# Kernel tuning notes

Measured on AMD Instinct MI355X. Metric: run time of the kernel, lower is better.

Reference implementation:

```python
import jax, jax.numpy as jnp
import numpy as np

B, S, L = 64, 512, 768


def setup_inputs() -> dict:
    key = jax.random.key(0)
    k1, k2 = jax.random.split(key)
    x = jax.random.normal(k1, (B, S, L), dtype=jnp.float32)
    # matches torch uniform_(-0.1, 0.1) init for the probe matrix b
    b = jax.random.uniform(k2, (L, L), minval=-0.1, maxval=0.1, dtype=jnp.float32)
    return {"x": x, "b": b}


def reference(x, b):
    # Original: z[b,i,j,h] = x_i - x_j; h = einsum('gh,bijh', b, z); dist = sum_g h^2
    # Identity: ||b @ (x_i - x_j)||^2 = ||p_i||^2 + ||p_j||^2 - 2 p_i . p_j,  p = x @ b^T
    p = jnp.einsum('gh,bsh->bsg', b, x)          # [B, S, L] projected points
    sq = jnp.sum(p * p, axis=-1)                 # [B, S]  squared norms
    gram = jnp.einsum('bsg,btg->bst', p, p)      # [B, S, S] inner products
    return sq[:, :, None] + sq[:, None, :] - 2.0 * gram  # [B, S, S]
```

## Files before the change

### kernel.cpp

```cpp
#include <hip/hip_runtime.h>
#include <hip/hip_bf16.h>


using bf16x8 = __attribute__((ext_vector_type(8))) __bf16;
using f32x4  = __attribute__((ext_vector_type(4))) float;
using fl4    = __attribute__((ext_vector_type(4))) float;
using u16x4  = __attribute__((ext_vector_type(4))) unsigned short;
using u32x4  = __attribute__((ext_vector_type(4))) unsigned int;

#define NB 64
#define NS 512
#define NL 768

__device__ __forceinline__ unsigned short f2bf(float f) {
  unsigned u = __builtin_bit_cast(unsigned, f);
  u += 0x7FFFu + ((u >> 16) & 1u);
  return (unsigned short)(u >> 16);
}

__device__ __forceinline__ void gload_lds16(const void* g, void* l) {
  __builtin_amdgcn_global_load_lds(
      (const __attribute__((address_space(1))) void*)g,
      (__attribute__((address_space(3))) void*)l, 16, 0, 0);
}

#define MEMFENCE asm volatile("" ::: "memory")

__global__ __launch_bounds__(256) void k_cvt_b(const float* __restrict__ b,
                                               unsigned short* __restrict__ bb) {
  const long t = (long)blockIdx.x * 256 + threadIdx.x;
  fl4 v = *(const fl4*)(b + t * 4);
  u16x4 o;
#pragma unroll
  for (int j = 0; j < 4; ++j) o[j] = f2bf(v[j]);
  *(u16x4*)(bb + t * 4) = o;
}

__global__ __launch_bounds__(256) void k_proj(const float* __restrict__ x,
                                              const unsigned short* __restrict__ bb,
                                              unsigned short* __restrict__ p) {
  __shared__ __align__(16) unsigned short smA[2][128 * 40];
  __shared__ __align__(16) unsigned short smB[2][128 * 32];
  const int tid = threadIdx.x;
  const int w = tid >> 6, l = tid & 63;
  const int wg = ((blockIdx.x & 7) * 192) + (blockIdx.x >> 3);
  const int nt = wg % 6, mt = wg / 6;
  const long m0 = (long)mt * 128, n0 = (long)nt * 128;
  const int wr = (w >> 1) * 64, wc = (w & 1) * 64;

  const int arow = tid >> 1, ah = tid & 1;
  const float* gA = x + (m0 + arow) * (long)NL + ah * 16;
  const int as_ = (arow >> 3) & 3;
  const int awr0 = arow * 80 + (((2 * ah + 0) ^ as_) << 4);
  const int awr1 = arow * 80 + (((2 * ah + 1) ^ as_) << 4);

  const int brow = tid >> 2;
  const int bcol = ((tid & 3) ^ ((brow >> 1) & 3)) * 8;
  const unsigned short* gB = bb + (n0 + brow) * (long)NL + bcol;

  const int qh = l >> 4, lr = l & 15;
  int aro[4];
#pragma unroll
  for (int m = 0; m < 4; ++m) {
    const int r = wr + m * 16 + lr;
    aro[m] = r * 80 + ((qh ^ ((r >> 3) & 3)) << 4);
  }
  const int boff = (wc + lr) * 64 + ((qh ^ ((lr >> 1) & 3)) << 4);

  f32x4 acc[4][4] = {};
  fl4 ar0, ar1, ar2, ar3;

#define ISSUE_B(k0, buf)                                                     \
  {                                                                          \
    char* d_ = (char*)&smB[buf][0] + w * 1024;                               \
    gload_lds16(gB + (k0), d_);                                              \
    gload_lds16(gB + (k0) + 64 * NL, d_ + 4096);                             \
  }
#define ISSUE_A(k0)                                                          \
  {                                                                          \
    ar0 = *(const fl4*)(gA + (k0));                                          \
    ar1 = *(const fl4*)(gA + (k0) + 4);                                      \
    ar2 = *(const fl4*)(gA + (k0) + 8);                                      \
    ar3 = *(const fl4*)(gA + (k0) + 12);                                     \
  }
#define WRITE_A(buf)                                                         \
  {                                                                          \
    unsigned q0, q1, q2, q3, q4, q5, q6, q7;                                 \
    asm("v_cvt_pk_bf16_f32 %0, %1, %2" : "=v"(q0) : "v"(ar0[0]), "v"(ar0[1]));\
    asm("v_cvt_pk_bf16_f32 %0, %1, %2" : "=v"(q1) : "v"(ar0[2]), "v"(ar0[3]));\
    asm("v_cvt_pk_bf16_f32 %0, %1, %2" : "=v"(q2) : "v"(ar1[0]), "v"(ar1[1]));\
    asm("v_cvt_pk_bf16_f32 %0, %1, %2" : "=v"(q3) : "v"(ar1[2]), "v"(ar1[3]));\
    asm("v_cvt_pk_bf16_f32 %0, %1, %2" : "=v"(q4) : "v"(ar2[0]), "v"(ar2[1]));\
    asm("v_cvt_pk_bf16_f32 %0, %1, %2" : "=v"(q5) : "v"(ar2[2]), "v"(ar2[3]));\
    asm("v_cvt_pk_bf16_f32 %0, %1, %2" : "=v"(q6) : "v"(ar3[0]), "v"(ar3[1]));\
    asm("v_cvt_pk_bf16_f32 %0, %1, %2" : "=v"(q7) : "v"(ar3[2]), "v"(ar3[3]));\
    u32x4 c0 = {q0, q1, q2, q3}, c1 = {q4, q5, q6, q7};                      \
    char* base_ = (char*)&smA[buf][0];                                       \
    *(u32x4*)(base_ + awr0) = c0;                                            \
    *(u32x4*)(base_ + awr1) = c1;                                            \
  }
#define COMPUTE(buf)                                                         \
  {                                                                          \
    const char* A_ = (const char*)&smA[buf][0];                              \
    const char* B_ = (const char*)&smB[buf][0];                              \
    bf16x8 fa[4], fb[4];                                                     \
    _Pragma("unroll")                                                        \
    for (int m = 0; m < 4; ++m) fa[m] = *(const bf16x8*)(A_ + aro[m]);       \
    _Pragma("unroll")                                                        \
    for (int n = 0; n < 4; ++n) fb[n] = *(const bf16x8*)(B_ + boff + n * 1024);\
    _Pragma("unroll")                                                        \
    for (int m = 0; m < 4; ++m)                                              \
      _Pragma("unroll")                                                      \
      for (int n = 0; n < 4; ++n)                                            \
        acc[m][n] = __builtin_amdgcn_mfma_f32_16x16x32_bf16(fa[m], fb[n],    \
                                                            acc[m][n], 0, 0, 0); \
  }

  ISSUE_B(0, 0)
  ISSUE_A(0)
  asm volatile("s_waitcnt vmcnt(0)" ::: "memory");
  WRITE_A(0)
  asm volatile("s_waitcnt lgkmcnt(0)" ::: "memory");
  __builtin_amdgcn_s_barrier();
  MEMFENCE;
  int cur = 0;
#pragma unroll 1
  for (int kt = 0; kt < 24; ++kt) {
    if (kt < 23) {
      ISSUE_B((kt + 1) * 32, cur ^ 1)
      ISSUE_A((kt + 1) * 32)
    }
    COMPUTE(cur)
    if (kt < 23) {
      asm volatile("s_waitcnt vmcnt(0)" ::: "memory");
      WRITE_A(cur ^ 1)
      asm volatile("s_waitcnt lgkmcnt(0)" ::: "memory");
      __builtin_amdgcn_s_barrier();
      MEMFENCE;
      cur ^= 1;
    }
  }
#undef ISSUE_B
#undef ISSUE_A
#undef WRITE_A
#undef COMPUTE

#pragma unroll
  for (int m = 0; m < 4; ++m) {
    const long rbase = m0 + wr + m * 16 + qh * 4;
#pragma unroll
    for (int n = 0; n < 4; ++n) {
      const long col = n0 + wc + n * 16 + lr;
#pragma unroll
      for (int r = 0; r < 4; ++r)
        p[(rbase + r) * NL + col] = f2bf(acc[m][n][r]);
    }
  }
}

__global__ __launch_bounds__(256) void k_sq(const unsigned short* __restrict__ p,
                                            float* __restrict__ sq) {
  const int row = blockIdx.x * 4 + (threadIdx.x >> 6);
  const int l = threadIdx.x & 63;
  const unsigned short* pr = p + (long)row * NL;
  float s = 0.f;
#pragma unroll
  for (int c = 0; c < 3; ++c) {
    u16x4 v = *(const u16x4*)(pr + (c * 64 + l) * 4);
#pragma unroll
    for (int j = 0; j < 4; ++j) {
      float f = __builtin_bit_cast(float, ((unsigned)v[j]) << 16);
      s += f * f;
    }
  }
#pragma unroll
  for (int d = 32; d >= 1; d >>= 1) s += __shfl_xor(s, d, 64);
  if (l == 0) sq[row] = s;
}

__global__ __launch_bounds__(256) void k_gram(const unsigned short* __restrict__ p,
                                              const float* __restrict__ sq,
                                              float* __restrict__ out) {
  __shared__ __align__(16) unsigned short smA[3][128 * 32];
  __shared__ __align__(16) unsigned short smB[3][128 * 32];
  const int tid = threadIdx.x;
  const int w = tid >> 6, l = tid & 63;
  const int wg = ((blockIdx.x & 7) * 128) + (blockIdx.x >> 3);
  const int batch = wg >> 4, tile = wg & 15;
  const int mt = tile >> 2, nt = tile & 3;
  const unsigned short* pb = p + (long)batch * NS * NL;
  const long m0 = (long)mt * 128, n0 = (long)nt * 128;
  const int wr = (w >> 1) * 64, wc = (w & 1) * 64;

  const int srow = tid >> 2;
  const int scol = ((tid & 3) ^ ((srow >> 1) & 3)) * 8;
  const unsigned short* gA = pb + (m0 + srow) * (long)NL + scol;
  const unsigned short* gB = pb + (n0 + srow) * (long)NL + scol;

  const int qh = l >> 4, lr = l & 15;
  const int aoff = (wr + lr) * 64 + ((qh ^ ((lr >> 1) & 3)) << 4);
  const int boff = (wc + lr) * 64 + ((qh ^ ((lr >> 1) & 3)) << 4);

  f32x4 acc[4][4] = {};

#define STAGE2(k0, buf)                                                      \
  {                                                                          \
    char* da_ = (char*)&smA[buf][0] + w * 1024;                              \
    char* db_ = (char*)&smB[buf][0] + w * 1024;                              \
    gload_lds16(gA + (k0), da_);                                             \
    gload_lds16(gA + (k0) + 64 * NL, da_ + 4096);                            \
    gload_lds16(gB + (k0), db_);                                             \
    gload_lds16(gB + (k0) + 64 * NL, db_ + 4096);                            \
  }
#define COMPUTE2(buf)                                                        \
  {                                                                          \
    const char* A_ = (const char*)&smA[buf][0];                              \
    const char* B_ = (const char*)&smB[buf][0];                              \
    bf16x8 fa[4], fb[4];                                                     \
    _Pragma("unroll")                                                        \
    for (int m = 0; m < 4; ++m)                                              \
      fa[m] = *(const bf16x8*)(A_ + aoff + m * 1024);                        \
    _Pragma("unroll")                                                        \
    for (int n = 0; n < 4; ++n)                                              \
      fb[n] = *(const bf16x8*)(B_ + boff + n * 1024);                        \
    _Pragma("unroll")                                                        \
    for (int m = 0; m < 4; ++m)                                              \
      _Pragma("unroll")                                                      \
      for (int n = 0; n < 4; ++n)                                            \
        acc[m][n] = __builtin_amdgcn_mfma_f32_16x16x32_bf16(fa[m], fb[n],    \
                                                            acc[m][n], 0, 0, 0); \
  }

  STAGE2(0, 0)
  STAGE2(32, 1)
  int cur = 0, nxt2 = 2;
#pragma unroll 1
  for (int kt = 0; kt < 23; ++kt) {
    asm volatile("s_waitcnt vmcnt(4)" ::: "memory");
    __builtin_amdgcn_s_barrier();
    MEMFENCE;
    if (kt < 22) STAGE2((kt + 2) * 32, nxt2)
    COMPUTE2(cur)
    cur = (cur == 2) ? 0 : cur + 1;
    nxt2 = (nxt2 == 2) ? 0 : nxt2 + 1;
  }
  asm volatile("s_waitcnt vmcnt(0)" ::: "memory");
  __builtin_amdgcn_s_barrier();
  MEMFENCE;
  COMPUTE2(cur)
#undef STAGE2
#undef COMPUTE2

  const float* sqb = sq + batch * NS;
  float* outb = out + (long)batch * NS * NS;
  float sqc[4];
#pragma unroll
  for (int n = 0; n < 4; ++n) sqc[n] = sqb[n0 + wc + n * 16 + lr];
#pragma unroll
  for (int m = 0; m < 4; ++m) {
#pragma unroll
    for (int r = 0; r < 4; ++r) {
      const long row = m0 + wr + m * 16 + qh * 4 + r;
      const float sr = sqb[row];
#pragma unroll
      for (int n = 0; n < 4; ++n) {
        const long col = n0 + wc + n * 16 + lr;
        outb[row * NS + col] = sr + sqc[n] - 2.0f * acc[m][n][r];
      }
    }
  }
}

extern "C" void kernel_launch(void* const* d_in, const int* in_sizes, int n_in,
                              void* d_out, int out_size, void* d_ws, size_t ws_size,
                              hipStream_t stream) {
  (void)in_sizes; (void)n_in; (void)out_size; (void)ws_size;
  const float* x = (const float*)d_in[0];
  const float* b = (const float*)d_in[1];
  float* out = (float*)d_out;
  char* ws = (char*)d_ws;
  unsigned short* bb = (unsigned short*)ws;
  float* sq          = (float*)(ws + 1179648);
  unsigned short* p  = (unsigned short*)(ws + 1310720);

  k_cvt_b<<<576, 256, 0, stream>>>(b, bb);
  k_proj <<<1536, 256, 0, stream>>>(x, bb, p);
  k_sq   <<<8192, 256, 0, stream>>>(p, sq);
  k_gram <<<1024, 256, 0, stream>>>(p, sq, out);
}
```

Measured before the change: 120.2 us.

## Pre-convert x to bf16 and use triple-buffered direct-to-LDS projection GEMM

Adds a separate pass that converts x from fp32 to bf16 in workspace. A new projection kernel then streams both bf16 operands straight into LDS with global_load_lds, using a three-stage buffer and swizzled layout. The old kernel converted fp32 x inside the GEMM. The aim is to cut the in-loop conversion and register staging and to deepen the load pipeline. The cost is an extra 50 MB write and read of bf16 x, and the new path only runs when the workspace is large enough.

After: 135.5 us. 1.13x slower.

```diff
diff --git a/kernel.cpp b/kernel.cpp
--- a/kernel.cpp
+++ b/kernel.cpp
@@ -34,6 +34,111 @@
 #pragma unroll
   for (int j = 0; j < 4; ++j) o[j] = f2bf(v[j]);
   *(u16x4*)(bb + t * 4) = o;
+}
+
+__global__ __launch_bounds__(256) void k_cvt_x(const float* __restrict__ x,
+                                               unsigned short* __restrict__ xb) {
+  const long t = (long)blockIdx.x * 256 + threadIdx.x;
+  const float* src = x + t * 16;
+  fl4 v0 = *(const fl4*)(src);
+  fl4 v1 = *(const fl4*)(src + 4);
+  fl4 v2 = *(const fl4*)(src + 8);
+  fl4 v3 = *(const fl4*)(src + 12);
+  u16x4 o0, o1, o2, o3;
+#pragma unroll
+  for (int j = 0; j < 4; ++j) {
+    o0[j] = f2bf(v0[j]); o1[j] = f2bf(v1[j]);
+    o2[j] = f2bf(v2[j]); o3[j] = f2bf(v3[j]);
+  }
+  unsigned short* dst = xb + t * 16;
+  *(u16x4*)(dst)      = o0;
+  *(u16x4*)(dst + 4)  = o1;
+  *(u16x4*)(dst + 8)  = o2;
+  *(u16x4*)(dst + 12) = o3;
+}
+
+__global__ __launch_bounds__(256) void k_projb(const unsigned short* __restrict__ xb,
+                                               const unsigned short* __restrict__ bb,
+                                               unsigned short* __restrict__ p) {
+  __shared__ __align__(16) unsigned short smA[3][128 * 32];
+  __shared__ __align__(16) unsigned short smB[3][128 * 32];
+  const int tid = threadIdx.x;
+  const int w = tid >> 6, l = tid & 63;
+  const int wg = ((blockIdx.x & 7) * 192) + (blockIdx.x >> 3);
+  const int nt = wg % 6, mt = wg / 6;
+  const long m0 = (long)mt * 128, n0 = (long)nt * 128;
+  const int wr = (w >> 1) * 64, wc = (w & 1) * 64;
+
+  const int srow = tid >> 2;
+  const int scol = ((tid & 3) ^ ((srow >> 1) & 3)) * 8;
+  const unsigned short* gA = xb + (m0 + srow) * (long)NL + scol;
+  const unsigned short* gB = bb + (n0 + srow) * (long)NL + scol;
+
+  const int qh = l >> 4, lr = l & 15;
+  const int aoff = (wr + lr) * 64 + ((qh ^ ((lr >> 1) & 3)) << 4);
+  const int boff = (wc + lr) * 64 + ((qh ^ ((lr >> 1) & 3)) << 4);
+
+  f32x4 acc[4][4] = {};
+
+#define STAGEP(k0, buf)                                                      \
+  {                                                                          \
+    char* da_ = (char*)&smA[buf][0] + w * 1024;                              \
+    char* db_ = (char*)&smB[buf][0] + w * 1024;                              \
+    gload_lds16(gA + (k0), da_);                                             \
+    gload_lds16(gA + (k0) + 64 * NL, da_ + 4096);                            \
+    gload_lds16(gB + (k0), db_);                                             \
+    gload_lds16(gB + (k0) + 64 * NL, db_ + 4096);                            \
+  }
+#define COMPUTEP(buf)                                                        \
+  {                                                                          \
+    const char* A_ = (const char*)&smA[buf][0];                              \
+    const char* B_ = (const char*)&smB[buf][0];                              \
+    bf16x8 fa[4], fb[4];                                                     \
+    _Pragma("unroll")                                                        \
+    for (int m = 0; m < 4; ++m)                                              \
+      fa[m] = *(const bf16x8*)(A_ + aoff + m * 1024);                        \
+    _Pragma("unroll")                                                        \
+    for (int n = 0; n < 4; ++n)                                              \
+      fb[n] = *(const bf16x8*)(B_ + boff + n * 1024);                        \
+    _Pragma("unroll")                                                        \
+    for (int m = 0; m < 4; ++m)                                              \
+      _Pragma("unroll")                                                      \
+      for (int n = 0; n < 4; ++n)                                            \
+        acc[m][n] = __builtin_amdgcn_mfma_f32_16x16x32_bf16(fa[m], fb[n],    \
+                                                            acc[m][n], 0, 0, 0); \
+  }
+
+  STAGEP(0, 0)
+  STAGEP(32, 1)
+  int cur = 0, nxt2 = 2;
+#pragma unroll 1
+  for (int kt = 0; kt < 23; ++kt) {
+    asm volatile("s_waitcnt vmcnt(4)" ::: "memory");
+    __builtin_amdgcn_s_barrier();
+    MEMFENCE;
+    if (kt < 22) STAGEP((kt + 2) * 32, nxt2)
+    COMPUTEP(cur)
+    cur = (cur == 2) ? 0 : cur + 1;
+    nxt2 = (nxt2 == 2) ? 0 : nxt2 + 1;
+  }
+  asm volatile("s_waitcnt vmcnt(0)" ::: "memory");
+  __builtin_amdgcn_s_barrier();
+  MEMFENCE;
+  COMPUTEP(cur)
+#undef STAGEP
+#undef COMPUTEP
+
+#pragma unroll
+  for (int m = 0; m < 4; ++m) {
+    const long rbase = m0 + wr + m * 16 + qh * 4;
+#pragma unroll
+    for (int n = 0; n < 4; ++n) {
+      const long col = n0 + wc + n * 16 + lr;
+#pragma unroll
+      for (int r = 0; r < 4; ++r)
+        p[(rbase + r) * NL + col] = f2bf(acc[m][n][r]);
+    }
+  }
 }
 
 __global__ __launch_bounds__(256) void k_proj(const float* __restrict__ x,
@@ -274,7 +379,7 @@
 extern "C" void kernel_launch(void* const* d_in, const int* in_sizes, int n_in,
                               void* d_out, int out_size, void* d_ws, size_t ws_size,
                               hipStream_t stream) {
-  (void)in_sizes; (void)n_in; (void)out_size; (void)ws_size;
+  (void)in_sizes; (void)n_in; (void)out_size;
   const float* x = (const float*)d_in[0];
   const float* b = (const float*)d_in[1];
   float* out = (float*)d_out;
@@ -282,9 +387,16 @@
   unsigned short* bb = (unsigned short*)ws;
   float* sq          = (float*)(ws + 1179648);
   unsigned short* p  = (unsigned short*)(ws + 1310720);
+  unsigned short* xb = (unsigned short*)(ws + 51642368);
+  const size_t need_xb = 51642368ull + 50331648ull;
 
   k_cvt_b<<<576, 256, 0, stream>>>(b, bb);
-  k_proj <<<1536, 256, 0, stream>>>(x, bb, p);
-  k_sq   <<<8192, 256, 0, stream>>>(p, sq);
-  k_gram <<<1024, 256, 0, stream>>>(p, sq, out);
-}
+  if (ws_size >= need_xb) {
+    k_cvt_x<<<6144, 256, 0, stream>>>(x, xb);
+    k_projb<<<1536, 256, 0, stream>>>(xb, bb, p);
+  } else {
+    k_proj<<<1536, 256, 0, stream>>>(x, bb, p);
+  }
+  k_sq  <<<8192, 256, 0, stream>>>(p, sq);
+  k_gram<<<1024, 256, 0, stream>>>(p, sq, out);
+}
```
